# Kernel tuning notes

Hardware: AMD Instinct MI355X
Metric: run time of the kernel (lower is better)

The kernel has to match this reference:

```python
import jax, jax.numpy as jnp
import numpy as np

TOP_K = 8


def setup_inputs() -> dict:
    key = jax.random.key(0)
    k1, k2 = jax.random.split(key)
    hidden_states = jax.random.normal(k1, (16384, 2048), dtype=jnp.float32)
    weight = jax.random.normal(k2, (64, 2048), dtype=jnp.float32) * 0.02
    return {"hidden_states": hidden_states, "weight": weight}


def reference(hidden_states, weight):
    # router_logits = F.linear(hidden_states, weight): [T, E]
    router_logits = jnp.einsum('th,eh->te', hidden_states, weight)
    # softmax in float32 as in the original
    router_probs = jax.nn.softmax(router_logits.astype(jnp.float32), axis=-1)
    router_top_values, router_indices = jax.lax.top_k(router_probs, TOP_K)
    # norm_topk_prob=True: renormalize selected probs to sum to 1
    router_top_values = router_top_values / jnp.sum(router_top_values, axis=-1, keepdims=True)
    return (router_logits,
            router_top_values.astype(hidden_states.dtype),
            router_indices)
```

## Files before the change

kernel.cpp:

```cpp
#include <hip/hip_runtime.h>
#include <math.h>

#define T_TOKENS 16384
#define HID      2048
#define NE       64
#define TOPK     8
#define TM       16
#define BK       128
#define NCH      (HID / BK)
#define RSTR     272
#define A_SPL    (TM * RSTR)
#define ABUF     (3 * A_SPL)
#define LDS_BYTES (2 * ABUF)

#define WS_SHORT8 49152

typedef float    f32x4  __attribute__((ext_vector_type(4)));
typedef short    short8 __attribute__((ext_vector_type(8)));
typedef unsigned uint4v __attribute__((ext_vector_type(4)));

#define MFMA16(A, B, C) __builtin_amdgcn_mfma_f32_16x16x32_bf16((A), (B), (C), 0, 0, 0)

static __device__ __forceinline__ unsigned short f2bf(float x) {
    unsigned u = __builtin_bit_cast(unsigned, x);
    return (unsigned short)((u + 0x7FFFu + ((u >> 16) & 1u)) >> 16);
}

static __device__ __forceinline__ void split8(const float4 v0, const float4 v1,
                                              uint4v& p0, uint4v& p1, uint4v& p2)
{
    const float x[8] = {v0.x, v0.y, v0.z, v0.w, v1.x, v1.y, v1.z, v1.w};
    #pragma unroll
    for (int j = 0; j < 4; ++j) {
        const float xe = x[2 * j], xo = x[2 * j + 1];
        const unsigned ue  = __builtin_bit_cast(unsigned, xe);
        const unsigned m0e = (ue + 0x8000u) & 0xFFFF0000u;
        const float    r1e = xe - __builtin_bit_cast(float, m0e);
        const unsigned u1e = __builtin_bit_cast(unsigned, r1e);
        const unsigned m1e = (u1e + 0x8000u) & 0xFFFF0000u;
        const float    r2e = r1e - __builtin_bit_cast(float, m1e);
        const unsigned u2e = __builtin_bit_cast(unsigned, r2e);
        const unsigned uo  = __builtin_bit_cast(unsigned, xo);
        const unsigned m0o = (uo + 0x8000u) & 0xFFFF0000u;
        const float    r1o = xo - __builtin_bit_cast(float, m0o);
        const unsigned u1o = __builtin_bit_cast(unsigned, r1o);
        const unsigned m1o = (u1o + 0x8000u) & 0xFFFF0000u;
        const float    r2o = r1o - __builtin_bit_cast(float, m1o);
        const unsigned u2o = __builtin_bit_cast(unsigned, r2o);
        p0[j] = m0o | (m0e >> 16);
        p1[j] = m1o | (m1e >> 16);
        p2[j] = (u2o & 0xFFFF0000u) | (u2e >> 16);
    }
}

__global__ __launch_bounds__(256) void split_weight_kernel(
    const float* __restrict__ weight, uint4v* __restrict__ ws)
{
    const int n = blockIdx.x;
    const int o = threadIdx.x;
    const float4 w0 = *(const float4*)&weight[(size_t)n * HID + o * 8];
    const float4 w1 = *(const float4*)&weight[(size_t)n * HID + o * 8 + 4];
    uint4v p0, p1, p2;
    split8(w0, w1, p0, p1, p2);
    const int t    = o >> 2;
    const int lane = (o & 3) * 16 + (n & 15);
    const int e    = n >> 4;
    const int base = t * 256 + e * 64 + lane;
    ws[base]         = p0;
    ws[base + 16384] = p1;
    ws[base + 32768] = p2;
}

__global__ __launch_bounds__(256, 4) void router_kernel(
    const float* __restrict__ hidden,
    const short8* __restrict__ bfrag,
    float* __restrict__ out_logits,
    float* __restrict__ out_vals,
    float* __restrict__ out_idxf)
{
    __shared__ __align__(16) char smem[LDS_BYTES];
    double (*lg)[NE + 1] = reinterpret_cast<double(*)[NE + 1]>(smem);

    const int tid  = threadIdx.x;
    const int tok0 = blockIdx.x * TM;
    const int lane = tid & 63;
    const int wave = tid >> 6;

    const int fr = lane & 15;
    const int fk = lane >> 4;

    int rowmap[4], colmap[4];
    {
        const unsigned short mb = f2bf((float)fr);
        const unsigned short ob = f2bf(0.03125f);
        short8 vm, vo;
        #pragma unroll
        for (int j = 0; j < 8; ++j) { vm[j] = (short)mb; vo[j] = (short)ob; }
        const f32x4 z = {0.f, 0.f, 0.f, 0.f};
        const f32x4 pr = MFMA16(vm, vo, z);
        const f32x4 pc = MFMA16(vo, vm, z);
        #pragma unroll
        for (int i = 0; i < 4; ++i) {
            rowmap[i] = (int)(pr[i] + 0.5f);
            colmap[i] = (int)(pc[i] + 0.5f);
        }
    }

    const int ar  = tid >> 4;
    const int ac8 = (tid & 15) * 8;
    const float* aG = hidden + (size_t)(tok0 + ar) * HID + ac8;
    const int aWOff = ar * RSTR + ac8 * 2;

    const short8* bP = bfrag + wave * 64 + lane;

    const int aOff = fr * RSTR + fk * 16;

    const f32x4 z4 = {0.f, 0.f, 0.f, 0.f};
    f32x4 acch = z4;
    f32x4 accl = z4;
    double accd[4] = {0, 0, 0, 0};

    float4 pa0, pa1;

    {
        pa0 = *(const float4*)(aG);
        pa1 = *(const float4*)(aG + 4);
        uint4v p0, p1, p2;
        split8(pa0, pa1, p0, p1, p2);
        char* aW = smem + aWOff;
        *(uint4v*)(aW            ) = p0;
        *(uint4v*)(aW +   A_SPL  ) = p1;
        *(uint4v*)(aW + 2*A_SPL  ) = p2;
    }
    __syncthreads();

    for (int c = 0; c < NCH; ++c) {
        const int cur = c & 1;
        const char* bufc = smem + cur * ABUF;

        if (c + 1 < NCH) {
            const int off = (c + 1) * BK;
            pa0 = *(const float4*)(aG + off);
            pa1 = *(const float4*)(aG + off + 4);
        }

        #pragma unroll
        for (int st = 0; st < 4; ++st) {
            const int t  = c * 4 + st;
            const int ao = aOff + st * 64;
            const short8 A0 = *(const short8*)(bufc + ao);
            const short8 A1 = *(const short8*)(bufc + A_SPL + ao);
            const short8 A2 = *(const short8*)(bufc + 2 * A_SPL + ao);
            const short8 B0 = bP[t * 256];
            const short8 B1 = bP[t * 256 + 16384];
            const short8 B2 = bP[t * 256 + 32768];
            acch = MFMA16(A0, B0, acch);
            accl = MFMA16(A0, B1, accl);
            accl = MFMA16(A1, B0, accl);
            accl = MFMA16(A1, B1, accl);
            accl = MFMA16(A0, B2, accl);
            accl = MFMA16(A2, B0, accl);
        }

        #pragma unroll
        for (int i = 0; i < 4; ++i) accd[i] += (double)acch[i];
        acch = z4;

        if (c + 1 < NCH) {
            uint4v p0, p1, p2;
            split8(pa0, pa1, p0, p1, p2);
            char* aW = smem + (cur ^ 1) * ABUF + aWOff;
            *(uint4v*)(aW            ) = p0;
            *(uint4v*)(aW +   A_SPL  ) = p1;
            *(uint4v*)(aW + 2*A_SPL  ) = p2;
        }
        __syncthreads();
    }

    #pragma unroll
    for (int i = 0; i < 4; ++i) {
        const int trow = rowmap[i];
        const int tok  = tok0 + trow;
        const int e0   = wave * 16 + colmap[i];
        const double l0 = accd[i] + (double)accl[i];
        out_logits[(size_t)tok * NE + e0] = (float)l0;
        lg[trow][e0] = l0;
    }
    __syncthreads();

    for (int tt = wave; tt < TM; tt += 4) {
        double cur = lg[tt][lane];
        double first = 0.0;
        float  s = 0.f, myv = 0.f;
        int myi = 0;
        #pragma unroll
        for (int i = 0; i < TOPK; ++i) {
            double mv = cur;
            #pragma unroll
            for (int off = 32; off; off >>= 1) {
                const double ov = __shfl_xor(mv, off);
                mv = ov > mv ? ov : mv;
            }
            const unsigned long long m = __ballot(cur == mv);
            const int mi = __ffsll(m) - 1;
            if (i == 0) first = mv;
            const float e = expf((float)(mv - first));
            s += e;
            if (lane == i)  { myv = e; myi = mi; }
            if (lane == mi) cur = -INFINITY;
        }
        if (lane < TOPK) {
            const int tok = tok0 + tt;
            out_vals[(size_t)tok * TOPK + lane] = myv / s;
            out_idxf[(size_t)tok * TOPK + lane] = (float)myi;
        }
    }
}

extern "C" void kernel_launch(void* const* d_in, const int* in_sizes, int n_in,
                              void* d_out, int out_size, void* d_ws, size_t ws_size,
                              hipStream_t stream) {
    const float* hidden = (const float*)d_in[0];
    const float* weight = (const float*)d_in[1];

    float* out        = (float*)d_out;
    float* out_logits = out;
    float* out_vals   = out + (size_t)T_TOKENS * NE;
    float* out_idxf   = out + (size_t)T_TOKENS * NE + (size_t)T_TOKENS * TOPK;

    uint4v* ws = (uint4v*)d_ws;

    hipLaunchKernelGGL(split_weight_kernel, dim3(NE), dim3(256), 0, stream,
                       weight, ws);
    hipLaunchKernelGGL(router_kernel, dim3(T_TOKENS / TM), dim3(256), 0, stream,
                       hidden, (const short8*)ws, out_logits, out_vals, out_idxf);
}
```

Before: 229.9 us.

## Double token tile per block to reuse B fragments and prefetch operands into registers

Each block now handles 32 tokens instead of 16. Each wave computes two 16-row MFMA fragments that share the same weight (B) fragments, which halves the global/L2 weight loads per token. The inner loop also software-pipelines the LDS A loads and global B loads one step ahead of the MFMAs. Each thread now loads 16 floats per chunk. In exchange, launch bounds drop to 2 blocks per SIMD, register pressure rises, LDS per block doubles, and the grid has half as many blocks, which lowers occupancy.

```diff
diff --git a/kernel.cpp b/kernel.cpp
--- a/kernel.cpp
+++ b/kernel.cpp
@@ -5,7 +5,7 @@
 #define HID      2048
 #define NE       64
 #define TOPK     8
-#define TM       16
+#define TM       32
 #define BK       128
 #define NCH      (HID / BK)
 #define RSTR     272
@@ -71,7 +71,7 @@
     ws[base + 32768] = p2;
 }
 
-__global__ __launch_bounds__(256, 4) void router_kernel(
+__global__ __launch_bounds__(256, 2) void router_kernel(
     const float* __restrict__ hidden,
     const short8* __restrict__ bfrag,
     float* __restrict__ out_logits,
@@ -106,85 +106,137 @@
         }
     }
 
-    const int ar  = tid >> 4;
-    const int ac8 = (tid & 15) * 8;
-    const float* aG = hidden + (size_t)(tok0 + ar) * HID + ac8;
-    const int aWOff = ar * RSTR + ac8 * 2;
+    const int ar   = tid >> 3;
+    const int ac16 = (tid & 7) * 16;
+    const float* aG = hidden + (size_t)(tok0 + ar) * HID + ac16;
+    const int aWOff = ar * RSTR + ac16 * 2;
 
     const short8* bP = bfrag + wave * 64 + lane;
 
-    const int aOff = fr * RSTR + fk * 16;
+    const int aOff0 = fr * RSTR + fk * 16;
+    const int aOff1 = (16 + fr) * RSTR + fk * 16;
 
     const f32x4 z4 = {0.f, 0.f, 0.f, 0.f};
-    f32x4 acch = z4;
-    f32x4 accl = z4;
-    double accd[4] = {0, 0, 0, 0};
-
-    float4 pa0, pa1;
+    f32x4 acch[2] = {z4, z4};
+    f32x4 accl[2] = {z4, z4};
+    double accd[2][4] = {{0, 0, 0, 0}, {0, 0, 0, 0}};
+
+    float4 pa[4];
+    short8 Bcur0, Bcur1, Bcur2;
 
     {
-        pa0 = *(const float4*)(aG);
-        pa1 = *(const float4*)(aG + 4);
+        #pragma unroll
+        for (int q = 0; q < 4; ++q) pa[q] = *(const float4*)(aG + 4 * q);
         uint4v p0, p1, p2;
-        split8(pa0, pa1, p0, p1, p2);
         char* aW = smem + aWOff;
+        split8(pa[0], pa[1], p0, p1, p2);
         *(uint4v*)(aW            ) = p0;
         *(uint4v*)(aW +   A_SPL  ) = p1;
         *(uint4v*)(aW + 2*A_SPL  ) = p2;
-    }
+        split8(pa[2], pa[3], p0, p1, p2);
+        *(uint4v*)(aW             + 16) = p0;
+        *(uint4v*)(aW +   A_SPL   + 16) = p1;
+        *(uint4v*)(aW + 2*A_SPL   + 16) = p2;
+    }
+    Bcur0 = bP[0];
+    Bcur1 = bP[16384];
+    Bcur2 = bP[32768];
     __syncthreads();
 
     for (int c = 0; c < NCH; ++c) {
-        const int cur = c & 1;
-        const char* bufc = smem + cur * ABUF;
+        const char* bufc = smem + (c & 1) * ABUF;
+
+        short8 A00 = *(const short8*)(bufc + aOff0);
+        short8 A01 = *(const short8*)(bufc + A_SPL + aOff0);
+        short8 A02 = *(const short8*)(bufc + 2 * A_SPL + aOff0);
+        short8 A10 = *(const short8*)(bufc + aOff1);
+        short8 A11 = *(const short8*)(bufc + A_SPL + aOff1);
+        short8 A12 = *(const short8*)(bufc + 2 * A_SPL + aOff1);
 
         if (c + 1 < NCH) {
             const int off = (c + 1) * BK;
-            pa0 = *(const float4*)(aG + off);
-            pa1 = *(const float4*)(aG + off + 4);
+            #pragma unroll
+            for (int q = 0; q < 4; ++q) pa[q] = *(const float4*)(aG + off + 4 * q);
         }
 
         #pragma unroll
         for (int st = 0; st < 4; ++st) {
-            const int t  = c * 4 + st;
-            const int ao = aOff + st * 64;
-            const short8 A0 = *(const short8*)(bufc + ao);
-            const short8 A1 = *(const short8*)(bufc + A_SPL + ao);
-            const short8 A2 = *(const short8*)(bufc + 2 * A_SPL + ao);
-            const short8 B0 = bP[t * 256];
-            const short8 B1 = bP[t * 256 + 16384];
-            const short8 B2 = bP[t * 256 + 32768];
-            acch = MFMA16(A0, B0, acch);
-            accl = MFMA16(A0, B1, accl);
-            accl = MFMA16(A1, B0, accl);
-            accl = MFMA16(A1, B1, accl);
-            accl = MFMA16(A0, B2, accl);
-            accl = MFMA16(A2, B0, accl);
-        }
-
-        #pragma unroll
-        for (int i = 0; i < 4; ++i) accd[i] += (double)acch[i];
-        acch = z4;
+            short8 An00, An01, An02, An10, An11, An12;
+            short8 Bn0, Bn1, Bn2;
+            if (st < 3) {
+                const int ao = (st + 1) * 64;
+                An00 = *(const short8*)(bufc + aOff0 + ao);
+                An01 = *(const short8*)(bufc + A_SPL + aOff0 + ao);
+                An02 = *(const short8*)(bufc + 2 * A_SPL + aOff0 + ao);
+                An10 = *(const short8*)(bufc + aOff1 + ao);
+                An11 = *(const short8*)(bufc + A_SPL + aOff1 + ao);
+                An12 = *(const short8*)(bufc + 2 * A_SPL + aOff1 + ao);
+                const int t = c * 4 + st + 1;
+                Bn0 = bP[t * 256];
+                Bn1 = bP[t * 256 + 16384];
+                Bn2 = bP[t * 256 + 32768];
+            } else if (c + 1 < NCH) {
+                const int t = (c + 1) * 4;
+                Bn0 = bP[t * 256];
+                Bn1 = bP[t * 256 + 16384];
+                Bn2 = bP[t * 256 + 32768];
+            }
+
+            acch[0] = MFMA16(A00, Bcur0, acch[0]);
+            accl[0] = MFMA16(A00, Bcur1, accl[0]);
+            accl[0] = MFMA16(A01, Bcur0, accl[0]);
+            accl[0] = MFMA16(A01, Bcur1, accl[0]);
+            accl[0] = MFMA16(A00, Bcur2, accl[0]);
+            accl[0] = MFMA16(A02, Bcur0, accl[0]);
+            acch[1] = MFMA16(A10, Bcur0, acch[1]);
+            accl[1] = MFMA16(A10, Bcur1, accl[1]);
+            accl[1] = MFMA16(A11, Bcur0, accl[1]);
+            accl[1] = MFMA16(A11, Bcur1, accl[1]);
+            accl[1] = MFMA16(A10, Bcur2, accl[1]);
+            accl[1] = MFMA16(A12, Bcur0, accl[1]);
+
+            if (st < 3) {
+                A00 = An00; A01 = An01; A02 = An02;
+                A10 = An10; A11 = An11; A12 = An12;
+                Bcur0 = Bn0; Bcur1 = Bn1; Bcur2 = Bn2;
+            } else if (c + 1 < NCH) {
+                Bcur0 = Bn0; Bcur1 = Bn1; Bcur2 = Bn2;
+            }
+        }
+
+        #pragma unroll
+        for (int f = 0; f < 2; ++f) {
+            #pragma unroll
+            for (int i = 0; i < 4; ++i) accd[f][i] += (double)acch[f][i];
+            acch[f] = z4;
+        }
 
         if (c + 1 < NCH) {
             uint4v p0, p1, p2;
-            split8(pa0, pa1, p0, p1, p2);
-            char* aW = smem + (cur ^ 1) * ABUF + aWOff;
+            char* aW = smem + ((c & 1) ^ 1) * ABUF + aWOff;
+            split8(pa[0], pa[1], p0, p1, p2);
             *(uint4v*)(aW            ) = p0;
             *(uint4v*)(aW +   A_SPL  ) = p1;
             *(uint4v*)(aW + 2*A_SPL  ) = p2;
+            split8(pa[2], pa[3], p0, p1, p2);
+            *(uint4v*)(aW             + 16) = p0;
+            *(uint4v*)(aW +   A_SPL   + 16) = p1;
+            *(uint4v*)(aW + 2*A_SPL   + 16) = p2;
         }
         __syncthreads();
     }
 
     #pragma unroll
-    for (int i = 0; i < 4; ++i) {
-        const int trow = rowmap[i];
-        const int tok  = tok0 + trow;
-        const int e0   = wave * 16 + colmap[i];
-        const double l0 = accd[i] + (double)accl[i];
-        out_logits[(size_t)tok * NE + e0] = (float)l0;
-        lg[trow][e0] = l0;
+    for (int f = 0; f < 2; ++f) {
+        #pragma unroll
+        for (int i = 0; i < 4; ++i) {
+            const int trow = f * 16 + rowmap[i];
+            const int tok  = tok0 + trow;
+            const int e0   = wave * 16 + colmap[i];
+            const double l0 = accd[f][i] + (double)accl[f][i];
+            out_logits[(size_t)tok * NE + e0] = (float)l0;
+            lg[trow][e0] = l0;
+        }
     }
     __syncthreads();
 
```

Measured after the change: 221.4 us. 3.7% less time.
